# Optimization experiments

Measured on AMD Instinct MI355X. Metric: run time of the kernel, lower is better.

## Reference

```python
import jax, jax.numpy as jnp
import numpy as np

N_NODES = 100000
N_EDGES = 1000000
D_FEAT = 64


def setup_inputs() -> dict:
    key = jax.random.key(0)
    k1, k2, k3 = jax.random.split(key, 3)
    embeddings = jax.random.normal(k1, (N_NODES, D_FEAT), dtype=jnp.float32)
    src = jax.random.randint(k2, (N_EDGES,), 0, N_NODES, dtype=jnp.int32)
    dst = jax.random.randint(k3, (N_EDGES,), 0, N_NODES, dtype=jnp.int32)
    return {"embeddings": embeddings, "src": src, "dst": dst}


def reference(embeddings, src, dst):
    # DGL update_all(copy_src('h','m'), mean('m','h')):
    # gather source features per edge, then mean-aggregate by destination.
    msgs = embeddings[src]                                    # [E, D]
    summed = jax.ops.segment_sum(msgs, dst, num_segments=N_NODES)   # [N, D]
    counts = jax.ops.segment_sum(jnp.ones((src.shape[0],), jnp.float32), dst,
                                 num_segments=N_NODES)        # [N]
    # nodes with no in-edges get 0 (DGL mean-of-empty semantics)
    denom = jnp.maximum(counts, 1.0)[:, None]
    return summed / denom
```

## Files before the change

kernel.cpp:

```cpp
#include <hip/hip_runtime.h>
#include <hip/hip_fp16.h>

#define N_NODES 100000
#define N_EDGES 1000000
#define D_FEAT  64

#define BIN_SHIFT 6
#define BIN_NODES 64
#define NBINS ((N_NODES + BIN_NODES - 1) >> BIN_SHIFT)
#define BIN_CAP 1152

#define NCHUNK 256
#define CHUNK_E ((N_EDGES + NCHUNK - 1) / NCHUNK)
#define PCHUNK 3968
#define CONV4 (N_NODES * D_FEAT / 4 / NCHUNK)

#define WS_PFCNT  0
#define WS_BUCKET (NCHUNK * NBINS)
#define WS_EMB16  (WS_BUCKET + NCHUNK * PCHUNK)
#define WS_NEEDED ((size_t)(WS_EMB16 + (size_t)N_NODES * D_FEAT / 2) * sizeof(int))

__global__ __launch_bounds__(1024) void prep_kernel(const float* __restrict__ emb,
                                                    const int* __restrict__ src,
                                                    const int* __restrict__ dst,
                                                    int* __restrict__ ws) {
    __shared__ int h[NBINS];
    int tid = threadIdx.x;
    int c   = blockIdx.x;
    for (int j = tid; j < NBINS; j += 1024) h[j] = 0;
    __syncthreads();

    int e0 = c * CHUNK_E, e1 = min(N_EDGES, e0 + CHUNK_E);
    for (int e = e0 + tid; e < e1; e += 1024)
        atomicAdd(&h[dst[e] >> BIN_SHIFT], 1);
    __syncthreads();

    int j0 = tid, j1 = tid + 1024;
    int c0 = (j0 < NBINS) ? h[j0] : 0;
    int c1 = (j1 < NBINS) ? h[j1] : 0;
    __syncthreads();

    if (tid < 64) {
        int lane = tid, carry = 0;
        for (int cb = 0; cb < NBINS; cb += 64) {
            int idx = cb + lane;
            int v = (idx < NBINS) ? h[idx] : 0;
            int incl = v;
            #pragma unroll
            for (int o = 1; o < 64; o <<= 1) {
                int t = __shfl_up(incl, o);
                if (lane >= o) incl += t;
            }
            if (idx < NBINS) h[idx] = carry + incl - v;
            carry += __shfl(incl, 63);
        }
    }
    __syncthreads();

    int* __restrict__ pfcnt = ws + WS_PFCNT + c * NBINS;
    if (j0 < NBINS) pfcnt[j0] = (h[j0] << 16) | c0;
    if (j1 < NBINS) pfcnt[j1] = (h[j1] << 16) | c1;

    int* __restrict__ run = ws + WS_BUCKET + c * PCHUNK;
    for (int e = e0 + tid; e < e1; e += 1024) {
        int d = dst[e], s = src[e];
        int slot = atomicAdd(&h[d >> BIN_SHIFT], 1);
        run[slot] = ((d & (BIN_NODES - 1)) << 17) | s;
    }

    {
        __half2* __restrict__ e16 = (__half2*)(ws + WS_EMB16);
        const float4* __restrict__ e32 = (const float4*)emb;
        int st = c * CONV4;
        for (int i = st + tid; i < st + CONV4; i += 1024) {
            float4 v = e32[i];
            e16[2 * i]     = __floats2half2_rn(v.x, v.y);
            e16[2 * i + 1] = __floats2half2_rn(v.z, v.w);
        }
    }
}

__global__ __launch_bounds__(512) void fused_gather_kernel(const int* __restrict__ ws,
                                                           float* __restrict__ out) {
    __shared__ int s_edges[BIN_CAP];
    __shared__ int s_sorted[BIN_CAP];
    __shared__ int s_rcnt[NCHUNK];
    __shared__ int s_roff[NCHUNK];
    __shared__ int s_rbase[NCHUNK];
    __shared__ int s_hist[BIN_NODES];
    __shared__ int s_off[BIN_NODES];
    __shared__ int s_cur[BIN_NODES];
    __shared__ int s_alloc;

    const char* __restrict__ emb16 = (const char*)(ws + WS_EMB16);
    int b   = blockIdx.x;
    int tid = threadIdx.x;

    if (tid < BIN_NODES) s_hist[tid] = 0;
    if (tid == 0) s_alloc = 0;
    __syncthreads();

    if (tid < NCHUNK) {
        unsigned pc = (unsigned)ws[WS_PFCNT + tid * NBINS + b];
        int cnt = (int)(pc & 0xFFFFu);
        int pf  = (int)(pc >> 16);
        s_rcnt[tid]  = cnt;
        s_rbase[tid] = tid * PCHUNK + pf;
        s_roff[tid]  = atomicAdd(&s_alloc, cnt);
    }
    __syncthreads();
    int total = s_alloc;
    if (total > BIN_CAP) total = BIN_CAP;

    {
        int g = tid >> 1, li = tid & 1;
        int cg = s_rcnt[g], og = s_roff[g];
        const int* __restrict__ run = ws + WS_BUCKET + s_rbase[g];
        for (int i = li; i < cg; i += 2) {
            int o = og + i;
            if (o < BIN_CAP) {
                int p = run[i];
                s_edges[o] = p;
                atomicAdd(&s_hist[p >> 17], 1);
            }
        }
    }
    __syncthreads();

    if (tid < 64) {
        int v = s_hist[tid];
        int incl = v;
        #pragma unroll
        for (int o = 1; o < 64; o <<= 1) {
            int t = __shfl_up(incl, o);
            if (tid >= o) incl += t;
        }
        s_off[tid] = incl - v;
        s_cur[tid] = incl - v;
    }
    __syncthreads();

    for (int i = tid; i < total; i += 512) {
        int p = s_edges[i];
        s_sorted[atomicAdd(&s_cur[p >> 17], 1)] = p & 0x1FFFF;
    }
    __syncthreads();

    int wave = tid >> 6, lane = tid & 63;
    int sub  = lane >> 4;
    int fq   = lane & 15;
    const int fb = fq << 3;

    #pragma unroll
    for (int pr = 0; pr < 4; ++pr) {
        int lnA = wave * 8 + pr * 2;
        int lnB = lnA + 1;
        int degA = s_hist[lnA], offA = s_off[lnA];
        int degB = s_hist[lnB], offB = s_off[lnB];

        float4 accA = make_float4(0.f, 0.f, 0.f, 0.f);
        float4 accB = make_float4(0.f, 0.f, 0.f, 0.f);

        int iA = sub, iB = sub;
        for (; iA + 12 < degA; iA += 16) {
            uint2 u0 = *(const uint2*)(emb16 + ((size_t)s_sorted[offA + iA]      << 7) + fb);
            uint2 u1 = *(const uint2*)(emb16 + ((size_t)s_sorted[offA + iA + 4]  << 7) + fb);
            uint2 u2 = *(const uint2*)(emb16 + ((size_t)s_sorted[offA + iA + 8]  << 7) + fb);
            uint2 u3 = *(const uint2*)(emb16 + ((size_t)s_sorted[offA + iA + 12] << 7) + fb);
            float2 f;
            f = __half22float2(*(__half2*)&u0.x); accA.x += f.x; accA.y += f.y;
            f = __half22float2(*(__half2*)&u0.y); accA.z += f.x; accA.w += f.y;
            f = __half22float2(*(__half2*)&u1.x); accA.x += f.x; accA.y += f.y;
            f = __half22float2(*(__half2*)&u1.y); accA.z += f.x; accA.w += f.y;
            f = __half22float2(*(__half2*)&u2.x); accA.x += f.x; accA.y += f.y;
            f = __half22float2(*(__half2*)&u2.y); accA.z += f.x; accA.w += f.y;
            f = __half22float2(*(__half2*)&u3.x); accA.x += f.x; accA.y += f.y;
            f = __half22float2(*(__half2*)&u3.y); accA.z += f.x; accA.w += f.y;
        }
        for (; iB + 12 < degB; iB += 16) {
            uint2 u0 = *(const uint2*)(emb16 + ((size_t)s_sorted[offB + iB]      << 7) + fb);
            uint2 u1 = *(const uint2*)(emb16 + ((size_t)s_sorted[offB + iB + 4]  << 7) + fb);
            uint2 u2 = *(const uint2*)(emb16 + ((size_t)s_sorted[offB + iB + 8]  << 7) + fb);
            uint2 u3 = *(const uint2*)(emb16 + ((size_t)s_sorted[offB + iB + 12] << 7) + fb);
            float2 f;
            f = __half22float2(*(__half2*)&u0.x); accB.x += f.x; accB.y += f.y;
            f = __half22float2(*(__half2*)&u0.y); accB.z += f.x; accB.w += f.y;
            f = __half22float2(*(__half2*)&u1.x); accB.x += f.x; accB.y += f.y;
            f = __half22float2(*(__half2*)&u1.y); accB.z += f.x; accB.w += f.y;
            f = __half22float2(*(__half2*)&u2.x); accB.x += f.x; accB.y += f.y;
            f = __half22float2(*(__half2*)&u2.y); accB.z += f.x; accB.w += f.y;
            f = __half22float2(*(__half2*)&u3.x); accB.x += f.x; accB.y += f.y;
            f = __half22float2(*(__half2*)&u3.y); accB.z += f.x; accB.w += f.y;
        }
        {
            uint2 a0 = make_uint2(0u, 0u), a1 = a0, a2 = a0;
            uint2 b0 = a0, b1 = a0, b2 = a0;
            if (iA < degA)     a0 = *(const uint2*)(emb16 + ((size_t)s_sorted[offA + iA]     << 7) + fb);
            if (iA + 4 < degA) a1 = *(const uint2*)(emb16 + ((size_t)s_sorted[offA + iA + 4] << 7) + fb);
            if (iA + 8 < degA) a2 = *(const uint2*)(emb16 + ((size_t)s_sorted[offA + iA + 8] << 7) + fb);
            if (iB < degB)     b0 = *(const uint2*)(emb16 + ((size_t)s_sorted[offB + iB]     << 7) + fb);
            if (iB + 4 < degB) b1 = *(const uint2*)(emb16 + ((size_t)s_sorted[offB + iB + 4] << 7) + fb);
            if (iB + 8 < degB) b2 = *(const uint2*)(emb16 + ((size_t)s_sorted[offB + iB + 8] << 7) + fb);
            float2 f;
            f = __half22float2(*(__half2*)&a0.x); accA.x += f.x; accA.y += f.y;
            f = __half22float2(*(__half2*)&a0.y); accA.z += f.x; accA.w += f.y;
            f = __half22float2(*(__half2*)&a1.x); accA.x += f.x; accA.y += f.y;
            f = __half22float2(*(__half2*)&a1.y); accA.z += f.x; accA.w += f.y;
            f = __half22float2(*(__half2*)&a2.x); accA.x += f.x; accA.y += f.y;
            f = __half22float2(*(__half2*)&a2.y); accA.z += f.x; accA.w += f.y;
            f = __half22float2(*(__half2*)&b0.x); accB.x += f.x; accB.y += f.y;
            f = __half22float2(*(__half2*)&b0.y); accB.z += f.x; accB.w += f.y;
            f = __half22float2(*(__half2*)&b1.x); accB.x += f.x; accB.y += f.y;
            f = __half22float2(*(__half2*)&b1.y); accB.z += f.x; accB.w += f.y;
            f = __half22float2(*(__half2*)&b2.x); accB.x += f.x; accB.y += f.y;
            f = __half22float2(*(__half2*)&b2.y); accB.z += f.x; accB.w += f.y;
        }

        #pragma unroll
        for (int m = 16; m < 64; m <<= 1) {
            accA.x += __shfl_xor(accA.x, m);  accB.x += __shfl_xor(accB.x, m);
            accA.y += __shfl_xor(accA.y, m);  accB.y += __shfl_xor(accB.y, m);
            accA.z += __shfl_xor(accA.z, m);  accB.z += __shfl_xor(accB.z, m);
            accA.w += __shfl_xor(accA.w, m);  accB.w += __shfl_xor(accB.w, m);
        }

        if (sub == 0) {
            int nodeA = (b << BIN_SHIFT) + lnA;
            int nodeB = (b << BIN_SHIFT) + lnB;
            float invA = 1.0f / (float)max(degA, 1);
            float invB = 1.0f / (float)max(degB, 1);
            accA.x *= invA; accA.y *= invA; accA.z *= invA; accA.w *= invA;
            accB.x *= invB; accB.y *= invB; accB.z *= invB; accB.w *= invB;
            if (nodeA < N_NODES)
                *(float4*)(out + (size_t)nodeA * D_FEAT + fq * 4) = accA;
            if (nodeB < N_NODES)
                *(float4*)(out + (size_t)nodeB * D_FEAT + fq * 4) = accB;
        }
    }
}


__global__ void gcn_zero_kernel(float* __restrict__ out, float* __restrict__ counts) {
    int stride = gridDim.x * blockDim.x;
    int i = blockIdx.x * blockDim.x + threadIdx.x;
    const int total = N_NODES * D_FEAT;
    for (int idx = i; idx < total; idx += stride) out[idx] = 0.0f;
    for (int idx = i; idx < N_NODES; idx += stride) counts[idx] = 0.0f;
}

__global__ void gcn_scatter_kernel(const float* __restrict__ emb,
                                   const int* __restrict__ src,
                                   const int* __restrict__ dst,
                                   float* __restrict__ out,
                                   float* __restrict__ counts) {
    int gid  = blockIdx.x * blockDim.x + threadIdx.x;
    int edge = gid >> 6;
    int lane = gid & 63;
    if (edge >= N_EDGES) return;
    int s = src[edge];
    int d = dst[edge];
    float v = emb[(size_t)s * D_FEAT + lane];
    atomicAdd(&out[(size_t)d * D_FEAT + lane], v);
    if (lane == 0) atomicAdd(&counts[d], 1.0f);
}

__global__ void gcn_norm_kernel(float* __restrict__ out,
                                const float* __restrict__ counts) {
    int i = blockIdx.x * blockDim.x + threadIdx.x;
    if (i >= N_NODES * D_FEAT) return;
    int n = i >> 6;
    float c = counts[n];
    out[i] *= (1.0f / fmaxf(c, 1.0f));
}


extern "C" void kernel_launch(void* const* d_in, const int* in_sizes, int n_in,
                              void* d_out, int out_size, void* d_ws, size_t ws_size,
                              hipStream_t stream) {
    const float* emb = (const float*)d_in[0];
    const int*   src = (const int*)d_in[1];
    const int*   dst = (const int*)d_in[2];
    float* out = (float*)d_out;

    if (ws_size >= WS_NEEDED) {
        int* ws = (int*)d_ws;
        prep_kernel<<<NCHUNK, 1024, 0, stream>>>(emb, src, dst, ws);
        fused_gather_kernel<<<NBINS, 512, 0, stream>>>(ws, out);
    } else {
        float* counts = (float*)d_ws;
        gcn_zero_kernel<<<2048, 256, 0, stream>>>(out, counts);
        const int scatter_blocks = (N_EDGES * 64) / 256;
        gcn_scatter_kernel<<<scatter_blocks, 256, 0, stream>>>(emb, src, dst, out, counts);
        const int norm_blocks = (N_NODES * D_FEAT + 255) / 256;
        gcn_norm_kernel<<<norm_blocks, 256, 0, stream>>>(out, counts);
    }
}
```

Baseline: 55.95 us.

## Split fp16 embedding table into feature slices and gather per-slice blocks

```diff
diff --git a/kernel.cpp b/kernel.cpp
--- a/kernel.cpp
+++ b/kernel.cpp
@@ -13,12 +13,15 @@
 #define NCHUNK 256
 #define CHUNK_E ((N_EDGES + NCHUNK - 1) / NCHUNK)
 #define PCHUNK 3968
-#define CONV4 (N_NODES * D_FEAT / 4 / NCHUNK)
+
+#define NSLICE 8
+#define SLICE_INTS (N_NODES * 4)
+#define SLICE_BYTES (N_NODES * 16)
 
 #define WS_PFCNT  0
 #define WS_BUCKET (NCHUNK * NBINS)
 #define WS_EMB16  (WS_BUCKET + NCHUNK * PCHUNK)
-#define WS_NEEDED ((size_t)(WS_EMB16 + (size_t)N_NODES * D_FEAT / 2) * sizeof(int))
+#define WS_NEEDED ((size_t)(WS_EMB16 + NSLICE * SLICE_INTS) * sizeof(int))
 
 __global__ __launch_bounds__(1024) void prep_kernel(const float* __restrict__ emb,
                                                     const int* __restrict__ src,
@@ -69,13 +72,22 @@
     }
 
     {
-        __half2* __restrict__ e16 = (__half2*)(ws + WS_EMB16);
+        int* __restrict__ e16 = ws + WS_EMB16;
         const float4* __restrict__ e32 = (const float4*)emb;
-        int st = c * CONV4;
-        for (int i = st + tid; i < st + CONV4; i += 1024) {
-            float4 v = e32[i];
-            e16[2 * i]     = __floats2half2_rn(v.x, v.y);
-            e16[2 * i + 1] = __floats2half2_rn(v.z, v.w);
+        const int CHUNKS = N_NODES * NSLICE / NCHUNK;
+        int k0 = c * CHUNKS;
+        for (int k = k0 + tid; k < k0 + CHUNKS; k += 1024) {
+            int n = k >> 3, f = k & 7;
+            float4 v0 = e32[n * 16 + f * 2];
+            float4 v1 = e32[n * 16 + f * 2 + 1];
+            __half2 h0 = __floats2half2_rn(v0.x, v0.y);
+            __half2 h1 = __floats2half2_rn(v0.z, v0.w);
+            __half2 h2 = __floats2half2_rn(v1.x, v1.y);
+            __half2 h3 = __floats2half2_rn(v1.z, v1.w);
+            uint4 u;
+            u.x = *(unsigned*)&h0; u.y = *(unsigned*)&h1;
+            u.z = *(unsigned*)&h2; u.w = *(unsigned*)&h3;
+            *(uint4*)(e16 + f * SLICE_INTS + n * 4) = u;
         }
     }
 }
@@ -92,9 +104,11 @@
     __shared__ int s_cur[BIN_NODES];
     __shared__ int s_alloc;
 
-    const char* __restrict__ emb16 = (const char*)(ws + WS_EMB16);
-    int b   = blockIdx.x;
-    int tid = threadIdx.x;
+    int b     = blockIdx.x >> 3;
+    int slice = blockIdx.x & 7;
+    int tid   = threadIdx.x;
+    const char* __restrict__ sl =
+        (const char*)(ws + WS_EMB16) + (size_t)slice * SLICE_BYTES;
 
     if (tid < BIN_NODES) s_hist[tid] = 0;
     if (tid == 0) s_alloc = 0;
@@ -147,94 +161,58 @@
     __syncthreads();
 
     int wave = tid >> 6, lane = tid & 63;
-    int sub  = lane >> 4;
-    int fq   = lane & 15;
-    const int fb = fq << 3;
+    int ln   = wave * 8 + (lane >> 3);
+    int es   = lane & 7;
+    int deg  = s_hist[ln];
+    int off  = s_off[ln];
+
+    float4 aLo = make_float4(0.f, 0.f, 0.f, 0.f);
+    float4 aHi = make_float4(0.f, 0.f, 0.f, 0.f);
+
+    int i = es;
+    for (; i + 8 < deg; i += 16) {
+        uint4 u0 = *(const uint4*)(sl + (size_t)s_sorted[off + i]     * 16);
+        uint4 u1 = *(const uint4*)(sl + (size_t)s_sorted[off + i + 8] * 16);
+        float2 f;
+        f = __half22float2(*(__half2*)&u0.x); aLo.x += f.x; aLo.y += f.y;
+        f = __half22float2(*(__half2*)&u0.y); aLo.z += f.x; aLo.w += f.y;
+        f = __half22float2(*(__half2*)&u0.z); aHi.x += f.x; aHi.y += f.y;
+        f = __half22float2(*(__half2*)&u0.w); aHi.z += f.x; aHi.w += f.y;
+        f = __half22float2(*(__half2*)&u1.x); aLo.x += f.x; aLo.y += f.y;
+        f = __half22float2(*(__half2*)&u1.y); aLo.z += f.x; aLo.w += f.y;
+        f = __half22float2(*(__half2*)&u1.z); aHi.x += f.x; aHi.y += f.y;
+        f = __half22float2(*(__half2*)&u1.w); aHi.z += f.x; aHi.w += f.y;
+    }
+    if (i < deg) {
+        uint4 u0 = *(const uint4*)(sl + (size_t)s_sorted[off + i] * 16);
+        float2 f;
+        f = __half22float2(*(__half2*)&u0.x); aLo.x += f.x; aLo.y += f.y;
+        f = __half22float2(*(__half2*)&u0.y); aLo.z += f.x; aLo.w += f.y;
+        f = __half22float2(*(__half2*)&u0.z); aHi.x += f.x; aHi.y += f.y;
+        f = __half22float2(*(__half2*)&u0.w); aHi.z += f.x; aHi.w += f.y;
+    }
 
     #pragma unroll
-    for (int pr = 0; pr < 4; ++pr) {
-        int lnA = wave * 8 + pr * 2;
-        int lnB = lnA + 1;
-        int degA = s_hist[lnA], offA = s_off[lnA];
-        int degB = s_hist[lnB], offB = s_off[lnB];
-
-        float4 accA = make_float4(0.f, 0.f, 0.f, 0.f);
-        float4 accB = make_float4(0.f, 0.f, 0.f, 0.f);
-
-        int iA = sub, iB = sub;
-        for (; iA + 12 < degA; iA += 16) {
-            uint2 u0 = *(const uint2*)(emb16 + ((size_t)s_sorted[offA + iA]      << 7) + fb);
-            uint2 u1 = *(const uint2*)(emb16 + ((size_t)s_sorted[offA + iA + 4]  << 7) + fb);
-            uint2 u2 = *(const uint2*)(emb16 + ((size_t)s_sorted[offA + iA + 8]  << 7) + fb);
-            uint2 u3 = *(const uint2*)(emb16 + ((size_t)s_sorted[offA + iA + 12] << 7) + fb);
-            float2 f;
-            f = __half22float2(*(__half2*)&u0.x); accA.x += f.x; accA.y += f.y;
-            f = __half22float2(*(__half2*)&u0.y); accA.z += f.x; accA.w += f.y;
-            f = __half22float2(*(__half2*)&u1.x); accA.x += f.x; accA.y += f.y;
-            f = __half22float2(*(__half2*)&u1.y); accA.z += f.x; accA.w += f.y;
-            f = __half22float2(*(__half2*)&u2.x); accA.x += f.x; accA.y += f.y;
-            f = __half22float2(*(__half2*)&u2.y); accA.z += f.x; accA.w += f.y;
-            f = __half22float2(*(__half2*)&u3.x); accA.x += f.x; accA.y += f.y;
-            f = __half22float2(*(__half2*)&u3.y); accA.z += f.x; accA.w += f.y;
-        }
-        for (; iB + 12 < degB; iB += 16) {
-            uint2 u0 = *(const uint2*)(emb16 + ((size_t)s_sorted[offB + iB]      << 7) + fb);
-            uint2 u1 = *(const uint2*)(emb16 + ((size_t)s_sorted[offB + iB + 4]  << 7) + fb);
-            uint2 u2 = *(const uint2*)(emb16 + ((size_t)s_sorted[offB + iB + 8]  << 7) + fb);
-            uint2 u3 = *(const uint2*)(emb16 + ((size_t)s_sorted[offB + iB + 12] << 7) + fb);
-            float2 f;
-            f = __half22float2(*(__half2*)&u0.x); accB.x += f.x; accB.y += f.y;
-            f = __half22float2(*(__half2*)&u0.y); accB.z += f.x; accB.w += f.y;
-            f = __half22float2(*(__half2*)&u1.x); accB.x += f.x; accB.y += f.y;
-            f = __half22float2(*(__half2*)&u1.y); accB.z += f.x; accB.w += f.y;
-            f = __half22float2(*(__half2*)&u2.x); accB.x += f.x; accB.y += f.y;
-            f = __half22float2(*(__half2*)&u2.y); accB.z += f.x; accB.w += f.y;
-            f = __half22float2(*(__half2*)&u3.x); accB.x += f.x; accB.y += f.y;
-            f = __half22float2(*(__half2*)&u3.y); accB.z += f.x; accB.w += f.y;
-        }
-        {
-            uint2 a0 = make_uint2(0u, 0u), a1 = a0, a2 = a0;
-            uint2 b0 = a0, b1 = a0, b2 = a0;
-            if (iA < degA)     a0 = *(const uint2*)(emb16 + ((size_t)s_sorted[offA + iA]     << 7) + fb);
-            if (iA + 4 < degA) a1 = *(const uint2*)(emb16 + ((size_t)s_sorted[offA + iA + 4] << 7) + fb);
-            if (iA + 8 < degA) a2 = *(const uint2*)(emb16 + ((size_t)s_sorted[offA + iA + 8] << 7) + fb);
-            if (iB < degB)     b0 = *(const uint2*)(emb16 + ((size_t)s_sorted[offB + iB]     << 7) + fb);
-            if (iB + 4 < degB) b1 = *(const uint2*)(emb16 + ((size_t)s_sorted[offB + iB + 4] << 7) + fb);
-            if (iB + 8 < degB) b2 = *(const uint2*)(emb16 + ((size_t)s_sorted[offB + iB + 8] << 7) + fb);
-            float2 f;
-            f = __half22float2(*(__half2*)&a0.x); accA.x += f.x; accA.y += f.y;
-            f = __half22float2(*(__half2*)&a0.y); accA.z += f.x; accA.w += f.y;
-            f = __half22float2(*(__half2*)&a1.x); accA.x += f.x; accA.y += f.y;
-            f = __half22float2(*(__half2*)&a1.y); accA.z += f.x; accA.w += f.y;
-            f = __half22float2(*(__half2*)&a2.x); accA.x += f.x; accA.y += f.y;
-            f = __half22float2(*(__half2*)&a2.y); accA.z += f.x; accA.w += f.y;
-            f = __half22float2(*(__half2*)&b0.x); accB.x += f.x; accB.y += f.y;
-            f = __half22float2(*(__half2*)&b0.y); accB.z += f.x; accB.w += f.y;
-            f = __half22float2(*(__half2*)&b1.x); accB.x += f.x; accB.y += f.y;
-            f = __half22float2(*(__half2*)&b1.y); accB.z += f.x; accB.w += f.y;
-            f = __half22float2(*(__half2*)&b2.x); accB.x += f.x; accB.y += f.y;
-            f = __half22float2(*(__half2*)&b2.y); accB.z += f.x; accB.w += f.y;
-        }
-
-        #pragma unroll
-        for (int m = 16; m < 64; m <<= 1) {
-            accA.x += __shfl_xor(accA.x, m);  accB.x += __shfl_xor(accB.x, m);
-            accA.y += __shfl_xor(accA.y, m);  accB.y += __shfl_xor(accB.y, m);
-            accA.z += __shfl_xor(accA.z, m);  accB.z += __shfl_xor(accB.z, m);
-            accA.w += __shfl_xor(accA.w, m);  accB.w += __shfl_xor(accB.w, m);
-        }
-
-        if (sub == 0) {
-            int nodeA = (b << BIN_SHIFT) + lnA;
-            int nodeB = (b << BIN_SHIFT) + lnB;
-            float invA = 1.0f / (float)max(degA, 1);
-            float invB = 1.0f / (float)max(degB, 1);
-            accA.x *= invA; accA.y *= invA; accA.z *= invA; accA.w *= invA;
-            accB.x *= invB; accB.y *= invB; accB.z *= invB; accB.w *= invB;
-            if (nodeA < N_NODES)
-                *(float4*)(out + (size_t)nodeA * D_FEAT + fq * 4) = accA;
-            if (nodeB < N_NODES)
-                *(float4*)(out + (size_t)nodeB * D_FEAT + fq * 4) = accB;
+    for (int m = 1; m < 8; m <<= 1) {
+        aLo.x += __shfl_xor(aLo.x, m);
+        aLo.y += __shfl_xor(aLo.y, m);
+        aLo.z += __shfl_xor(aLo.z, m);
+        aLo.w += __shfl_xor(aLo.w, m);
+        aHi.x += __shfl_xor(aHi.x, m);
+        aHi.y += __shfl_xor(aHi.y, m);
+        aHi.z += __shfl_xor(aHi.z, m);
+        aHi.w += __shfl_xor(aHi.w, m);
+    }
+
+    if (es == 0) {
+        int node = (b << BIN_SHIFT) + ln;
+        if (node < N_NODES) {
+            float inv = 1.0f / (float)max(deg, 1);
+            aLo.x *= inv; aLo.y *= inv; aLo.z *= inv; aLo.w *= inv;
+            aHi.x *= inv; aHi.y *= inv; aHi.z *= inv; aHi.w *= inv;
+            float* orow = out + (size_t)node * D_FEAT + slice * 8;
+            *(float4*)(orow)     = aLo;
+            *(float4*)(orow + 4) = aHi;
         }
     }
 }
@@ -285,7 +263,7 @@
     if (ws_size >= WS_NEEDED) {
         int* ws = (int*)d_ws;
         prep_kernel<<<NCHUNK, 1024, 0, stream>>>(emb, src, dst, ws);
-        fused_gather_kernel<<<NBINS, 512, 0, stream>>>(ws, out);
+        fused_gather_kernel<<<NBINS * NSLICE, 512, 0, stream>>>(ws, out);
     } else {
         float* counts = (float*)d_ws;
         gcn_zero_kernel<<<2048, 256, 0, stream>>>(out, counts);
```

New measurement: 117.5 us. 110% more time.
